# Kernel optimization log

Hardware: AMD Instinct MI355X
Metric: run time of the kernel (lower is better)

## Reference

```python
import jax, jax.numpy as jnp
import numpy as np

N_HEADS = 16
COS_SIM_SCALE = 8.0  # lucidrains flash_cosine_sim_attention default temperature
RMS_EPS = 1e-6
ROPE_THETA = 10000.0


def _rms_norm(t, g):
    # RMSNorm over head dim with learnable gain (QKNorm)
    return t * jax.lax.rsqrt(jnp.mean(t * t, axis=-1, keepdims=True) + RMS_EPS) * g


def _rotate_half(x):
    d = x.shape[-1]
    return jnp.concatenate([-x[..., d // 2:], x[..., : d // 2]], axis=-1)


def _image_rope_cos_sin(n, d, dtype):
    # 2D axial RoPE: first half of head dim encodes row position, second half column.
    side = int(np.sqrt(n))
    assert side * side == n, 'ImageRoPE expects a square token grid'
    n_freq = d // 4
    freqs = 1.0 / (ROPE_THETA ** (jnp.arange(n_freq, dtype=jnp.float32) / n_freq))
    pos = jnp.arange(side, dtype=jnp.float32)
    grid_h = jnp.repeat(pos, side)   # (n,) row index
    grid_w = jnp.tile(pos, side)     # (n,) col index
    ang_h = grid_h[:, None] * freqs  # (n, d//4)
    ang_w = grid_w[:, None] * freqs  # (n, d//4)
    # rotate-half convention: angles for dims [0:d//2] paired with [d//2:d]
    ang = jnp.concatenate([ang_h, ang_w], axis=-1)          # (n, d//2)
    ang = jnp.concatenate([ang, ang], axis=-1)              # (n, d)
    return jnp.cos(ang).astype(dtype), jnp.sin(ang).astype(dtype)


def setup_inputs() -> dict:
    key = jax.random.key(0)
    ks = jax.random.split(key, 6)
    b, n, dm = 8, 1024, 1024
    h = N_HEADS
    d = dm // h
    s = 1.0 / np.sqrt(dm)
    return {
        'x': jax.random.normal(ks[0], (b, n, dm), dtype=jnp.float32),
        'w_qkv': jax.random.normal(ks[1], (dm, 3 * dm), dtype=jnp.float32) * s,
        'b_qkv': jnp.zeros((3 * dm,), dtype=jnp.float32),
        'q_gain': jnp.ones((d,), dtype=jnp.float32),
        'k_gain': jnp.ones((d,), dtype=jnp.float32),
        'w_out': jax.random.normal(ks[2], (dm, dm), dtype=jnp.float32) * s,
        'b_out': jnp.zeros((dm,), dtype=jnp.float32),
    }


def reference(x, w_qkv, b_qkv, q_gain, k_gain, w_out, b_out):
    b, n, dm = x.shape
    h = N_HEADS
    d = dm // h
    qkv = x @ w_qkv + b_qkv                       # (b, n, 3*dm)
    qkv = qkv.reshape(b, n, 3, h, d)
    qkv = jnp.transpose(qkv, (2, 0, 3, 1, 4))     # (3, b, h, n, d)
    q, k, v = qkv[0], qkv[1], qkv[2]
    # QK-norm (RMSNorm over head dim)
    q = _rms_norm(q, q_gain)
    k = _rms_norm(k, k_gain)
    # 2D image RoPE
    cos, sin = _image_rope_cos_sin(n, d, x.dtype)
    q = q * cos + _rotate_half(q) * sin
    k = k * cos + _rotate_half(k) * sin
    # cosine-sim attention: l2-normalize q,k, fixed scale, softmax, weighted sum
    q = q / jnp.linalg.norm(q, axis=-1, keepdims=True)
    k = k / jnp.linalg.norm(k, axis=-1, keepdims=True)
    scores = jnp.einsum('bhnd,bhmd->bhnm', q, k) * COS_SIM_SCALE
    attn = jax.nn.softmax(scores, axis=-1)
    o = jnp.einsum('bhnm,bhmd->bhnd', attn, v)    # (b, h, n, d)
    o = jnp.transpose(o, (0, 2, 1, 3)).reshape(b, n, dm)
    return o @ w_out + b_out
```

## Files before the change

kernel.cpp:

```cpp
#include <hip/hip_runtime.h>
#include <hip/hip_bf16.h>
#include <cstdint>

typedef __bf16 bf16;
typedef __bf16 bf16x8 __attribute__((ext_vector_type(8)));
typedef __bf16 bf16x4 __attribute__((ext_vector_type(4)));
typedef float f32x4 __attribute__((ext_vector_type(4)));

__device__ inline bf16x8 cvt8(const float* __restrict__ p) {
  float4 a = *(const float4*)p;
  float4 b = *(const float4*)(p + 4);
  bf16x8 r;
  r[0] = (bf16)a.x; r[1] = (bf16)a.y; r[2] = (bf16)a.z; r[3] = (bf16)a.w;
  r[4] = (bf16)b.x; r[5] = (bf16)b.y; r[6] = (bf16)b.z; r[7] = (bf16)b.w;
  return r;
}

__device__ inline void gl_lds16(const bf16* g, bf16* l) {
  auto gp = reinterpret_cast<const __attribute__((address_space(1))) uint32_t*>(
      reinterpret_cast<uintptr_t>(g));
  auto lp = reinterpret_cast<__attribute__((address_space(3))) uint32_t*>(
      reinterpret_cast<uintptr_t>(l));
  __builtin_amdgcn_global_load_lds(gp, lp, 16, 0, 0);
}

#define BAR() asm volatile("s_barrier" ::: "memory")

__global__ __launch_bounds__(256) void prep_k(const float* __restrict__ x,
                                              bf16* __restrict__ xb,
                                              const float* __restrict__ wqkv,
                                              bf16* __restrict__ wqkvT,
                                              const float* __restrict__ wo,
                                              bf16* __restrict__ woT) {
  __shared__ bf16 T[32][33];
  const int bid = blockIdx.x;
  if (bid < 4096) {
    long i = ((long)bid * 256 + threadIdx.x) * 8;
    *(bf16x8*)(xb + i) = cvt8(x + i);
    return;
  }
  const float* in;
  bf16* out;
  int R, C, bx, by;
  if (bid < 7168) {
    int t = bid - 4096;
    in = wqkv; out = wqkvT; R = 1024; C = 3072;
    bx = t % 96; by = t / 96;
  } else {
    int t = bid - 7168;
    in = wo; out = woT; R = 1024; C = 1024;
    bx = t % 32; by = t / 32;
  }
  int tc = bx * 32, tr = by * 32;
  int c = threadIdx.x & 31, r8 = threadIdx.x >> 5;
#pragma unroll
  for (int i = 0; i < 4; i++) {
    int r = r8 + i * 8;
    T[r][c] = (bf16)in[(long)(tr + r) * C + tc + c];
  }
  __syncthreads();
#pragma unroll
  for (int i = 0; i < 4; i++) {
    int r = r8 + i * 8;
    out[(long)(tc + r) * R + tr + c] = T[c][r];
  }
}

__global__ __launch_bounds__(512, 4) void gemm256(const bf16* __restrict__ A,
                                                  const bf16* __restrict__ Bt,
                                                  const float* __restrict__ bias,
                                                  int K,
                                                  bf16* __restrict__ qb,
                                                  bf16* __restrict__ kb,
                                                  bf16* __restrict__ v4,
                                                  const float* __restrict__ qg,
                                                  const float* __restrict__ kg) {
  __shared__ __align__(16) bf16 As[2][4096];
  __shared__ __align__(16) bf16 Bs[2][8192];

  const int tid = threadIdx.x;
  const int lane = tid & 63;
  const int w = tid >> 6;
  const int quad = lane >> 4;
  const int l16 = lane & 15;
  const int wr = w >> 2;
  const int wc = w & 3;

  const int gx = gridDim.x;
  const int bid = blockIdx.y * gx + blockIdx.x;
  const int cpx = (gx * gridDim.y) >> 3;
  const int sw = (bid & 7) * cpx + (bid >> 3);
  const int n0 = (sw % gx) * 256;
  const int m0 = (sw / gx) * 128;

  const int srA = tid >> 2;
  const int scS = ((tid & 3) ^ ((tid >> 3) & 3)) * 8;
  const bf16* aS = A + (long)(m0 + srA) * K + scS;
  const bf16* bS0 = Bt + (long)(n0 + srA) * K + scS;
  const bf16* bS1 = bS0 + (long)128 * K;

#define STAGE(tb, kt1)                                                   \
  {                                                                      \
    const long kc = (long)(kt1)*32;                                      \
    gl_lds16(aS + kc, &As[tb][w * 512]);                                 \
    gl_lds16(bS0 + kc, &Bs[tb][w * 512]);                                \
    gl_lds16(bS1 + kc, &Bs[tb][4096 + w * 512]);                         \
  }

  const int cphys = (quad ^ ((l16 >> 1) & 3)) * 8;
  const int aoff = (wr * 64 + l16) * 32 + cphys;
  const int boff = (wc * 64 + l16) * 32 + cphys;

  f32x4 acc[4][4];
#pragma unroll
  for (int i = 0; i < 4; i++)
#pragma unroll
    for (int j = 0; j < 4; j++) acc[i][j] = f32x4{0.f, 0.f, 0.f, 0.f};

  const int NK = K >> 5;
  STAGE(0, 0);

  for (int kt = 0; kt < NK; ++kt) {
    const int pb = kt & 1;
    const int tb = pb ^ 1;
    const bool pf = (kt + 1 < NK);
    if (pf) {
      STAGE(tb, kt + 1);
      asm volatile("s_waitcnt vmcnt(3)" ::: "memory");
    } else {
      asm volatile("s_waitcnt vmcnt(0)" ::: "memory");
    }
    BAR();
    bf16x8 afr[4], bfr[4];
#pragma unroll
    for (int n = 0; n < 4; n++) bfr[n] = *(const bf16x8*)&Bs[pb][boff + n * 512];
#pragma unroll
    for (int m = 0; m < 4; m++) afr[m] = *(const bf16x8*)&As[pb][aoff + m * 512];
    __builtin_amdgcn_s_setprio(1);
#pragma unroll
    for (int m = 0; m < 4; m++)
#pragma unroll
      for (int n = 0; n < 4; n++)
        acc[m][n] = __builtin_amdgcn_mfma_f32_16x16x32_bf16(afr[m], bfr[n], acc[m][n], 0, 0, 0);
    __builtin_amdgcn_s_setprio(0);
    BAR();
  }

  const int which = n0 >> 10;
  if (which == 2) {
    const int T0 = (((m0 & 1023) + wr * 64) >> 2) + quad;
    const int bh = (m0 >> 10) * 16 + (((n0 + wc * 64) & 1023) >> 6);
#pragma unroll
    for (int m = 0; m < 4; m++) {
#pragma unroll
      for (int n = 0; n < 4; n++) {
        int ng = n0 + wc * 64 + n * 16 + l16;
        int dc = n * 16 + l16;
        float bj = bias[ng];
        bf16x4 pv;
#pragma unroll
        for (int r = 0; r < 4; r++) pv[r] = (bf16)(acc[m][n][r] + bj);
        *(bf16x4*)(v4 + ((long)bh * 16384 + (long)(T0 + m * 4) * 64 + dc) * 4) = pv;
      }
    }
    return;
  }

  const float* gg = which ? kg : qg;
  bf16* dst = which ? kb : qb;
  const float fold = which ? 1.0f : 8.0f;
  const int h = ((n0 + wc * 64) & 1023) >> 6;
  const int bh = (m0 >> 10) * 16 + h;
  float bj[4], gain[4];
#pragma unroll
  for (int j = 0; j < 4; j++) {
    bj[j] = bias[n0 + wc * 64 + j * 16 + l16];
    gain[j] = gg[j * 16 + l16];
  }
  const float f = exp2f((float)l16 * (-13.287712379549449f / 16.0f));

#pragma unroll
  for (int m = 0; m < 4; m++) {
#pragma unroll
    for (int r = 0; r < 4; r++) {
      int ntok = (m0 & 1023) + wr * 64 + m * 16 + quad * 4 + r;
      float v0 = acc[m][0][r] + bj[0];
      float v1 = acc[m][1][r] + bj[1];
      float v2 = acc[m][2][r] + bj[2];
      float v3 = acc[m][3][r] + bj[3];
      float ss = v0 * v0 + v1 * v1 + v2 * v2 + v3 * v3;
#pragma unroll
      for (int mk = 1; mk <= 8; mk <<= 1) ss += __shfl_xor(ss, mk, 64);
      float rms = rsqrtf(ss * (1.0f / 64.0f) + 1e-6f);
      v0 *= rms * gain[0]; v1 *= rms * gain[1]; v2 *= rms * gain[2]; v3 *= rms * gain[3];
      float sh, ch_, swv, cw;
      __sincosf((float)(ntok >> 5) * f, &sh, &ch_);
      __sincosf((float)(ntok & 31) * f, &swv, &cw);
      float w0 = v0 * ch_ - v2 * sh;
      float w1 = v1 * cw - v3 * swv;
      float w2 = v2 * ch_ + v0 * sh;
      float w3 = v3 * cw + v1 * swv;
      float nn = w0 * w0 + w1 * w1 + w2 * w2 + w3 * w3;
#pragma unroll
      for (int mk = 1; mk <= 8; mk <<= 1) nn += __shfl_xor(nn, mk, 64);
      float inv = rsqrtf(nn) * fold;
      long base = ((long)bh * 1024 + ntok) * 64 + l16;
      dst[base] = (bf16)(w0 * inv);
      dst[base + 16] = (bf16)(w1 * inv);
      dst[base + 32] = (bf16)(w2 * inv);
      dst[base + 48] = (bf16)(w3 * inv);
    }
  }
}

__global__ __launch_bounds__(256, 4) void gemm_bt1(const bf16* __restrict__ A,
                                                   const bf16* __restrict__ Bt,
                                                   const float* __restrict__ bias,
                                                   int N, int K,
                                                   float* __restrict__ out) {
  __shared__ __align__(16) bf16 As[2][4096];
  __shared__ __align__(16) bf16 Bs[2][4096];

  const int tid = threadIdx.x;
  const int lane = tid & 63;
  const int w = tid >> 6;
  const int wm = (w & 1) * 64;
  const int wn = (w >> 1) * 64;
  const int quad = lane >> 4;
  const int l16 = lane & 15;

  const int m0 = blockIdx.y * 128;
  const int n0 = blockIdx.x * 128;

  int srow[2], scof[2];
#pragma unroll
  for (int l = 0; l < 2; l++) {
    int s = l * 256 + tid;
    srow[l] = s >> 2;
    scof[l] = ((s & 3) ^ ((s >> 3) & 3)) * 8;
  }

  auto stage = [&](int tb, int k0) {
    int hh = k0 >> 6;
#pragma unroll
    for (int l = 0; l < 2; l++) {
      int m1 = m0 + srow[l];
      int dc = (k0 & 63) + scof[l];
      const bf16* ga = A + ((long)((m1 >> 10) * 16 + hh) * 1024 + (m1 & 1023)) * 64 + dc;
      gl_lds16(ga, &As[tb][l * 2048 + w * 512]);
      gl_lds16(Bt + (long)(n0 + srow[l]) * K + k0 + scof[l], &Bs[tb][l * 2048 + w * 512]);
    }
  };

  const int cphys = (quad ^ ((l16 >> 1) & 3)) * 8;

  f32x4 acc[4][4];
#pragma unroll
  for (int i = 0; i < 4; i++)
#pragma unroll
    for (int j = 0; j < 4; j++) acc[i][j] = f32x4{0.f, 0.f, 0.f, 0.f};

  const int NK = K >> 5;
  stage(0, 0);

  for (int kt = 0; kt < NK; ++kt) {
    const int pb = kt & 1;
    const int tb = pb ^ 1;
    const bool pf = (kt + 1 < NK);
    if (pf) {
      stage(tb, (kt + 1) << 5);
      asm volatile("s_waitcnt vmcnt(4)" ::: "memory");
    } else {
      asm volatile("s_waitcnt vmcnt(0)" ::: "memory");
    }
    BAR();
    bf16x8 af[4], bfr[4];
#pragma unroll
    for (int i = 0; i < 4; i++) {
      af[i] = *(const bf16x8*)&As[pb][(wm + i * 16 + l16) * 32 + cphys];
      bfr[i] = *(const bf16x8*)&Bs[pb][(wn + i * 16 + l16) * 32 + cphys];
    }
    __builtin_amdgcn_s_setprio(1);
#pragma unroll
    for (int i = 0; i < 4; i++)
#pragma unroll
      for (int j = 0; j < 4; j++)
        acc[i][j] = __builtin_amdgcn_mfma_f32_16x16x32_bf16(af[i], bfr[j], acc[i][j], 0, 0, 0);
    __builtin_amdgcn_s_setprio(0);
    BAR();
  }

#pragma unroll
  for (int i = 0; i < 4; i++)
#pragma unroll
    for (int j = 0; j < 4; j++)
#pragma unroll
      for (int r = 0; r < 4; r++) {
        int mg = m0 + wm + i * 16 + quad * 4 + r;
        int ng = n0 + wn + j * 16 + l16;
        out[(long)mg * N + ng] = acc[i][j][r] + bias[ng];
      }
}

__global__ __launch_bounds__(256, 2) void attn_k(bf16* __restrict__ qb,
                                                 const bf16* __restrict__ kb,
                                                 const bf16* __restrict__ v4) {
  __shared__ __align__(16) bf16 Ks[2][64][72];
  __shared__ __align__(16) bf16 Vl[2][4096];
  __shared__ __align__(16) bf16 Ps[4][2][16][72];

  const int tid = threadIdx.x;
  const int lane = tid & 63;
  const int w = tid >> 6;
  const int quad = lane >> 4;
  const int l16 = lane & 15;

  const int bh = blockIdx.y;
  const int q0 = blockIdx.x * 256 + w * 64;

  bf16x8 aq[4][2];
  long qrow[4];
#pragma unroll
  for (int g = 0; g < 4; g++) {
    qrow[g] = ((long)bh * 1024 + q0 + g * 16 + l16) * 64;
    aq[g][0] = *(const bf16x8*)(qb + qrow[g] + quad * 8);
    aq[g][1] = *(const bf16x8*)(qb + qrow[g] + 32 + quad * 8);
  }

  f32x4 o[4][4];
#pragma unroll
  for (int g = 0; g < 4; g++)
#pragma unroll
    for (int i = 0; i < 4; i++) o[g][i] = f32x4{0.f, 0.f, 0.f, 0.f};
  float ls[4] = {0.f, 0.f, 0.f, 0.f};

  const int sr = tid >> 3, sc = (tid & 7) * 8;
  const bf16* kbase = kb + (long)bh * 65536;
  const bf16* vbase = v4 + (long)bh * 65536;

  bf16x8 kr0 = *(const bf16x8*)(kbase + (long)sr * 64 + sc);
  bf16x8 kr1 = *(const bf16x8*)(kbase + (long)(sr + 32) * 64 + sc);
  gl_lds16(vbase + (w * 2) * 512 + lane * 8, &Vl[0][(w * 2) * 512]);
  gl_lds16(vbase + (w * 2 + 1) * 512 + lane * 8, &Vl[0][(w * 2 + 1) * 512]);
  asm volatile("s_waitcnt vmcnt(0)" ::: "memory");
  *(bf16x8*)&Ks[0][sr][sc] = kr0;
  *(bf16x8*)&Ks[0][sr + 32][sc] = kr1;
  asm volatile("s_waitcnt lgkmcnt(0)" ::: "memory");
  BAR();

  for (int kt = 0; kt < 1024; kt += 64) {
    const int cur = (kt >> 6) & 1;
    const bool pf = (kt + 64 < 1024);
    if (pf) {
      kr0 = *(const bf16x8*)(kbase + (long)(kt + 64 + sr) * 64 + sc);
      kr1 = *(const bf16x8*)(kbase + (long)(kt + 64 + sr + 32) * 64 + sc);
      gl_lds16(vbase + (long)(kt + 64) * 64 + (w * 2) * 512 + lane * 8,
               &Vl[cur ^ 1][(w * 2) * 512]);
      gl_lds16(vbase + (long)(kt + 64) * 64 + (w * 2 + 1) * 512 + lane * 8,
               &Vl[cur ^ 1][(w * 2 + 1) * 512]);
    }

    bf16x8 kf[4][2], vf[4][2];
#pragma unroll
    for (int i = 0; i < 4; i++) {
      kf[i][0] = *(const bf16x8*)&Ks[cur][i * 16 + l16][quad * 8];
      kf[i][1] = *(const bf16x8*)&Ks[cur][i * 16 + l16][32 + quad * 8];
      int D4 = (i * 16 + l16) * 4;
      bf16x4 a0 = *(const bf16x4*)&Vl[cur][quad * 512 + D4];
      bf16x4 a1 = *(const bf16x4*)&Vl[cur][quad * 512 + D4 + 256];
      bf16x4 a2 = *(const bf16x4*)&Vl[cur][quad * 512 + D4 + 2048];
      bf16x4 a3 = *(const bf16x4*)&Vl[cur][quad * 512 + D4 + 2048 + 256];
      vf[i][0] = __builtin_shufflevector(a0, a1, 0, 1, 2, 3, 4, 5, 6, 7);
      vf[i][1] = __builtin_shufflevector(a2, a3, 0, 1, 2, 3, 4, 5, 6, 7);
    }

    bf16x8 bp[2][2];
#pragma unroll
    for (int g = 0; g < 4; g++) {
      const int sl = g & 1;
#pragma unroll
      for (int i = 0; i < 4; i++) {
        f32x4 st = f32x4{0.f, 0.f, 0.f, 0.f};
        st = __builtin_amdgcn_mfma_f32_16x16x32_bf16(kf[i][0], aq[g][0], st, 0, 0, 0);
        st = __builtin_amdgcn_mfma_f32_16x16x32_bf16(kf[i][1], aq[g][1], st, 0, 0, 0);
        bf16x4 pk;
#pragma unroll
        for (int r = 0; r < 4; r++) {
          float p = __expf(st[r] - 8.0f);
          ls[g] += p;
          pk[r] = (bf16)p;
        }
        *(bf16x4*)&Ps[w][sl][l16][i * 16 + quad * 4] = pk;
      }
      bp[sl][0] = *(const bf16x8*)&Ps[w][sl][l16][quad * 8];
      bp[sl][1] = *(const bf16x8*)&Ps[w][sl][l16][32 + quad * 8];
      if (g > 0) {
        const int pg = (g - 1) & 1;
#pragma unroll
        for (int i = 0; i < 4; i++) {
          o[g - 1][i] = __builtin_amdgcn_mfma_f32_16x16x32_bf16(vf[i][0], bp[pg][0], o[g - 1][i], 0, 0, 0);
          o[g - 1][i] = __builtin_amdgcn_mfma_f32_16x16x32_bf16(vf[i][1], bp[pg][1], o[g - 1][i], 0, 0, 0);
        }
      }
    }
#pragma unroll
    for (int i = 0; i < 4; i++) {
      o[3][i] = __builtin_amdgcn_mfma_f32_16x16x32_bf16(vf[i][0], bp[1][0], o[3][i], 0, 0, 0);
      o[3][i] = __builtin_amdgcn_mfma_f32_16x16x32_bf16(vf[i][1], bp[1][1], o[3][i], 0, 0, 0);
    }

    if (pf) {
      asm volatile("s_waitcnt vmcnt(0)" ::: "memory");
      *(bf16x8*)&Ks[cur ^ 1][sr][sc] = kr0;
      *(bf16x8*)&Ks[cur ^ 1][sr + 32][sc] = kr1;
    }
    asm volatile("s_waitcnt lgkmcnt(0)" ::: "memory");
    BAR();
  }

#pragma unroll
  for (int g = 0; g < 4; g++) {
    float l = ls[g];
    l += __shfl_xor(l, 16, 64);
    l += __shfl_xor(l, 32, 64);
    float inv = 1.0f / l;
#pragma unroll
    for (int i = 0; i < 4; i++) {
      bf16x4 ov;
#pragma unroll
      for (int r = 0; r < 4; r++) ov[r] = (bf16)(o[g][i][r] * inv);
      *(bf16x4*)(qb + qrow[g] + i * 16 + quad * 4) = ov;
    }
  }
}

extern "C" void kernel_launch(void* const* d_in, const int* in_sizes, int n_in,
                              void* d_out, int out_size, void* d_ws, size_t ws_size,
                              hipStream_t stream) {
  (void)in_sizes; (void)n_in; (void)out_size; (void)ws_size;
  const float* x     = (const float*)d_in[0];
  const float* w_qkv = (const float*)d_in[1];
  const float* b_qkv = (const float*)d_in[2];
  const float* q_g   = (const float*)d_in[3];
  const float* k_g   = (const float*)d_in[4];
  const float* w_out = (const float*)d_in[5];
  const float* b_out = (const float*)d_in[6];
  float* out = (float*)d_out;

  char* ws = (char*)d_ws;
  bf16* wqkvT = (bf16*)ws; ws += (long)3072 * 1024 * 2;
  bf16* woT   = (bf16*)ws; ws += (long)1024 * 1024 * 2;
  bf16* xb    = (bf16*)ws; ws += (long)8192 * 1024 * 2;
  bf16* qb    = (bf16*)ws; ws += (long)128 * 1024 * 64 * 2;
  bf16* kb    = (bf16*)ws; ws += (long)128 * 1024 * 64 * 2;
  bf16* v4    = (bf16*)ws; ws += (long)128 * 64 * 1024 * 2;

  prep_k<<<8192, 256, 0, stream>>>(x, xb, w_qkv, wqkvT, w_out, woT);
  gemm256<<<dim3(3072 / 256, 8192 / 128), 512, 0, stream>>>(xb, wqkvT, b_qkv, 1024,
                                                            qb, kb, v4, q_g, k_g);
  attn_k<<<dim3(4, 128), 256, 0, stream>>>(qb, kb, v4);
  gemm_bt1<<<dim3(1024 / 128, 8192 / 128), 256, 0, stream>>>(qb, woT, b_out,
                                                             1024, 1024, out);
}
```

Baseline: 246.0 us.

## Software-pipeline GEMM main loops with register fragment prefetch and a single barrier

```diff
diff --git a/kernel.cpp b/kernel.cpp
--- a/kernel.cpp
+++ b/kernel.cpp
@@ -111,6 +111,14 @@
   const int aoff = (wr * 64 + l16) * 32 + cphys;
   const int boff = (wc * 64 + l16) * 32 + cphys;
 
+#define LOADFRAGS(pb)                                                          \
+  {                                                                            \
+    _Pragma("unroll") for (int n = 0; n < 4; n++) bfr[n] =                     \
+        *(const bf16x8*)&Bs[pb][boff + n * 512];                               \
+    _Pragma("unroll") for (int m = 0; m < 4; m++) afr[m] =                     \
+        *(const bf16x8*)&As[pb][aoff + m * 512];                               \
+  }
+
   f32x4 acc[4][4];
 #pragma unroll
   for (int i = 0; i < 4; i++)
@@ -118,24 +126,15 @@
     for (int j = 0; j < 4; j++) acc[i][j] = f32x4{0.f, 0.f, 0.f, 0.f};
 
   const int NK = K >> 5;
+  bf16x8 afr[4], bfr[4];
+
   STAGE(0, 0);
+  asm volatile("s_waitcnt vmcnt(0)" ::: "memory");
+  BAR();
+  LOADFRAGS(0);
+  STAGE(1, 1);
 
   for (int kt = 0; kt < NK; ++kt) {
-    const int pb = kt & 1;
-    const int tb = pb ^ 1;
-    const bool pf = (kt + 1 < NK);
-    if (pf) {
-      STAGE(tb, kt + 1);
-      asm volatile("s_waitcnt vmcnt(3)" ::: "memory");
-    } else {
-      asm volatile("s_waitcnt vmcnt(0)" ::: "memory");
-    }
-    BAR();
-    bf16x8 afr[4], bfr[4];
-#pragma unroll
-    for (int n = 0; n < 4; n++) bfr[n] = *(const bf16x8*)&Bs[pb][boff + n * 512];
-#pragma unroll
-    for (int m = 0; m < 4; m++) afr[m] = *(const bf16x8*)&As[pb][aoff + m * 512];
     __builtin_amdgcn_s_setprio(1);
 #pragma unroll
     for (int m = 0; m < 4; m++)
@@ -143,7 +142,12 @@
       for (int n = 0; n < 4; n++)
         acc[m][n] = __builtin_amdgcn_mfma_f32_16x16x32_bf16(afr[m], bfr[n], acc[m][n], 0, 0, 0);
     __builtin_amdgcn_s_setprio(0);
-    BAR();
+    if (kt + 1 < NK) {
+      asm volatile("s_waitcnt vmcnt(0)" ::: "memory");
+      BAR();
+      LOADFRAGS((kt + 1) & 1);
+      if (kt + 2 < NK) STAGE(kt & 1, kt + 2);
+    }
   }
 
   const int which = n0 >> 10;
@@ -261,25 +265,23 @@
     for (int j = 0; j < 4; j++) acc[i][j] = f32x4{0.f, 0.f, 0.f, 0.f};
 
   const int NK = K >> 5;
+  bf16x8 af[4], bfr[4];
+
+#define LOADFRAGS1(pb)                                                         \
+  {                                                                            \
+    _Pragma("unroll") for (int i = 0; i < 4; i++) {                            \
+      af[i] = *(const bf16x8*)&As[pb][(wm + i * 16 + l16) * 32 + cphys];       \
+      bfr[i] = *(const bf16x8*)&Bs[pb][(wn + i * 16 + l16) * 32 + cphys];      \
+    }                                                                          \
+  }
+
   stage(0, 0);
+  asm volatile("s_waitcnt vmcnt(0)" ::: "memory");
+  BAR();
+  LOADFRAGS1(0);
+  stage(1, 32);
 
   for (int kt = 0; kt < NK; ++kt) {
-    const int pb = kt & 1;
-    const int tb = pb ^ 1;
-    const bool pf = (kt + 1 < NK);
-    if (pf) {
-      stage(tb, (kt + 1) << 5);
-      asm volatile("s_waitcnt vmcnt(4)" ::: "memory");
-    } else {
-      asm volatile("s_waitcnt vmcnt(0)" ::: "memory");
-    }
-    BAR();
-    bf16x8 af[4], bfr[4];
-#pragma unroll
-    for (int i = 0; i < 4; i++) {
-      af[i] = *(const bf16x8*)&As[pb][(wm + i * 16 + l16) * 32 + cphys];
-      bfr[i] = *(const bf16x8*)&Bs[pb][(wn + i * 16 + l16) * 32 + cphys];
-    }
     __builtin_amdgcn_s_setprio(1);
 #pragma unroll
     for (int i = 0; i < 4; i++)
@@ -287,7 +289,12 @@
       for (int j = 0; j < 4; j++)
         acc[i][j] = __builtin_amdgcn_mfma_f32_16x16x32_bf16(af[i], bfr[j], acc[i][j], 0, 0, 0);
     __builtin_amdgcn_s_setprio(0);
-    BAR();
+    if (kt + 1 < NK) {
+      asm volatile("s_waitcnt vmcnt(0)" ::: "memory");
+      BAR();
+      LOADFRAGS1((kt + 1) & 1);
+      if (kt + 2 < NK) stage(kt & 1, (kt + 2) << 5);
+    }
   }
 
 #pragma unroll
```

Result: no change. 241.7 us (median of 2 runs) (-1.7%).
